# Performance work log

Hardware: AMD Instinct MI355X
Metric: run time of the kernel (lower is better)

The kernel has to match this reference:

```python
import jax, jax.numpy as jnp
import numpy as np

DIM = 1024
H = 16
HD = DIM // H
SCALE = HD ** -0.5
LAMBDA_INIT = 0.1
EPS = 1e-6


def setup_inputs() -> dict:
    key0 = jax.random.key(0)
    ks = jax.random.split(key0, 12)
    B, Nq, Nk = 2, 1024, 2048
    w = 0.02
    inp = {
        "query": jax.random.normal(ks[0], (B, Nq, DIM), jnp.float32),
        "key": jax.random.normal(ks[1], (B, Nk, DIM), jnp.float32),
        "value": jax.random.normal(ks[2], (B, Nk, DIM), jnp.float32),
        "qpos": jax.random.randint(ks[3], (B, Nq), 0, Nq, jnp.int32),
        "kpos": jax.random.randint(ks[4], (B, Nk), 0, Nk, jnp.int32),
        "q1_w": jax.random.normal(ks[5], (DIM, DIM), jnp.float32) * w,
        "q2_w": jax.random.normal(ks[6], (DIM, DIM), jnp.float32) * w,
        "kv1_w": jax.random.normal(ks[7], (2 * DIM, DIM), jnp.float32) * w,
        "kv2_w": jax.random.normal(ks[8], (2 * DIM, DIM), jnp.float32) * w,
        "proj_w": jax.random.normal(ks[9], (DIM, DIM), jnp.float32) * w,
        "proj_b": jnp.zeros((DIM,), jnp.float32),
        "norm_w": jnp.ones((DIM,), jnp.float32),
        "lambda_1": jnp.ones((1, H, 1, 1), jnp.float32),
        # layer_idx=0, max_layer=12 -> scale = 1/12
        "lambda_2": jnp.full((1, H, 1, 1), 1.0 - LAMBDA_INIT * (1.0 / 12.0), jnp.float32),
    }
    return inp


def _split_heads(x, B, N):
    # [B, N, DIM] -> [B, H, N, HD]
    return x.reshape(B, N, H, HD).transpose(0, 2, 1, 3)


def reference(query, key, value, qpos, kpos, q1_w, q2_w, kv1_w, kv2_w,
              proj_w, proj_b, norm_w, lambda_1, lambda_2):
    B, Nq, C = query.shape
    Nk = key.shape[1]

    q1 = _split_heads(query @ q1_w.T, B, Nq)
    q2 = _split_heads(query @ q2_w.T, B, Nq)

    kv1 = (key @ kv1_w.T).reshape(B, Nk, 2, H, HD).transpose(2, 0, 3, 1, 4)
    k1, v1 = kv1[0], kv1[1]  # [B, H, Nk, HD]
    kv2 = (key @ kv2_w.T).reshape(B, Nk, 2, H, HD).transpose(2, 0, 3, 1, 4)
    k2 = kv2[0]

    attn1 = jax.nn.softmax(jnp.einsum('bhqd,bhkd->bhqk', q1, k1) * SCALE, axis=-1)
    attn2 = jax.nn.softmax(jnp.einsum('bhqd,bhkd->bhqk', q2, k2) * SCALE, axis=-1)

    lambda_full = lambda_1 - lambda_2 + LAMBDA_INIT  # [1, H, 1, 1]
    diff_attn = attn1 - lambda_full * attn2

    x = jnp.einsum('bhqk,bhkd->bhqd', diff_attn, v1)
    x = x.transpose(0, 2, 1, 3).reshape(B, Nq, C)

    # RMSNorm (computed in float32 like the original)
    xf = x.astype(jnp.float32)
    xf = xf * jax.lax.rsqrt(jnp.mean(xf * xf, axis=-1, keepdims=True) + EPS) * norm_w
    x = xf.astype(x.dtype)

    return x @ proj_w.T + proj_b
```

## Files before the change

kernel.cpp:

```cpp
#include <hip/hip_runtime.h>
#include <cstdint>

typedef unsigned short u16;
typedef __bf16 bf16x8 __attribute__((ext_vector_type(8)));
typedef float f32x4 __attribute__((ext_vector_type(4)));
typedef float f32x16 __attribute__((ext_vector_type(16)));
typedef uint32_t u32x4 __attribute__((ext_vector_type(4)));

#define SCALE_LOG2E (0.125f * 1.44269504088896340736f)

__device__ __forceinline__ u16 f2bf(float f) {
    uint32_t u = __builtin_bit_cast(uint32_t, f);
    u += 0x7fff + ((u >> 16) & 1);
    return (u16)(u >> 16);
}
__device__ __forceinline__ float bf2f(u16 u) {
    return __builtin_bit_cast(float, (uint32_t)u << 16);
}

__device__ __forceinline__ void gload_lds16(const void* g, void* l) {
    __builtin_amdgcn_global_load_lds(
        (__attribute__((address_space(1))) void*)g,
        (__attribute__((address_space(3))) void*)l, 16, 0, 0);
}

__global__ __launch_bounds__(256) void cvt_all(const float* __restrict__ s0,
                                               const float* __restrict__ s1,
                                               const float* __restrict__ s2,
                                               const float* __restrict__ s3,
                                               const float* __restrict__ s4,
                                               const float* __restrict__ s5,
                                               const float* __restrict__ s6,
                                               u16* __restrict__ d0, u16* __restrict__ d1,
                                               u16* __restrict__ d2, u16* __restrict__ d3,
                                               u16* __restrict__ d4) {
    int i = blockIdx.x * 256 + threadIdx.x;
    const float* src;
    u16* dst;
    int off;
    if (i < 524288)       { src = s0; dst = d0; off = i; }
    else if (i < 1572864) { src = s1; dst = d1; off = i - 524288; }
    else if (i < 1835008) { src = s2; dst = d2; off = i - 1572864; }
    else if (i < 2097152) { src = s3; dst = d2 + (size_t)1024 * 1024; off = i - 1835008; }
    else if (i < 2621440) { src = s4; dst = d3; off = i - 2097152; }
    else if (i < 2883584) { src = s5; dst = d3 + (size_t)2048 * 1024; off = i - 2621440; }
    else                  { src = s6; dst = d4; off = i - 2883584; }
    float4 v = ((const float4*)src)[off];
    ushort4 o;
    o.x = f2bf(v.x); o.y = f2bf(v.y); o.z = f2bf(v.z); o.w = f2bf(v.w);
    ((ushort4*)dst)[off] = o;
}

__global__ __launch_bounds__(256) void gemm_qkv(const u16* __restrict__ Xq,
                                                const u16* __restrict__ Wq,
                                                const u16* __restrict__ Xk,
                                                const u16* __restrict__ Wkv,
                                                u16* __restrict__ q1s, u16* __restrict__ q2s,
                                                u16* __restrict__ k1s, u16* __restrict__ v1t,
                                                u16* __restrict__ k2s) {
    __shared__ u16 As[128 * 32];
    __shared__ u16 Bs[128 * 32];
    const int K = 1024;
    const int bid = blockIdx.x;
    int mode, bm, bn;
    const u16 *A, *B;
    if (bid < 256) {
        mode = 0; bm = bid >> 4; bn = bid & 15; A = Xq; B = Wq;
    } else {
        int t = bid - 256;
        mode = 1; bm = t / 24; bn = t % 24; A = Xk; B = Wkv;
    }
    const int tid = threadIdx.x;
    const int l = tid & 63, w = tid >> 6;
    const int c = l & 15, g = l >> 4;
    const int wr = w >> 1, wc = w & 1;

    f32x4 acc[4][4];
#pragma unroll
    for (int i = 0; i < 4; i++)
#pragma unroll
        for (int j = 0; j < 4; j++) acc[i][j] = f32x4{0.f, 0.f, 0.f, 0.f};

    const u16* Abase = A + (size_t)(bm * 128) * K;
    const u16* Bbase = B + (size_t)(bn * 128) * K;
    const int r0 = 32 * w + (l >> 2);
    const int ch = (l & 3) * 8;

    for (int kb = 0; kb < K; kb += 32) {
        gload_lds16(Abase + (size_t)r0 * K + kb + ch,        As + 32 * w * 32);
        gload_lds16(Abase + (size_t)(r0 + 16) * K + kb + ch, As + (32 * w + 16) * 32);
        gload_lds16(Bbase + (size_t)r0 * K + kb + ch,        Bs + 32 * w * 32);
        gload_lds16(Bbase + (size_t)(r0 + 16) * K + kb + ch, Bs + (32 * w + 16) * 32);
        __syncthreads();
        bf16x8 af[4], bfr[4];
#pragma unroll
        for (int mi = 0; mi < 4; mi++)
            af[mi] = *(const bf16x8*)&As[(64 * wr + 16 * mi + c) * 32 + 8 * g];
#pragma unroll
        for (int ni = 0; ni < 4; ni++)
            bfr[ni] = *(const bf16x8*)&Bs[(64 * wc + 16 * ni + c) * 32 + 8 * g];
#pragma unroll
        for (int mi = 0; mi < 4; mi++)
#pragma unroll
            for (int ni = 0; ni < 4; ni++)
                acc[mi][ni] = __builtin_amdgcn_mfma_f32_16x16x32_bf16(
                    af[mi], bfr[ni], acc[mi][ni], 0, 0, 0);
        __syncthreads();
    }

#pragma unroll
    for (int mi = 0; mi < 4; mi++)
#pragma unroll
        for (int ni = 0; ni < 4; ni++)
#pragma unroll
            for (int j = 0; j < 4; j++) {
                int m = bm * 128 + 64 * wr + 16 * mi + 4 * g + j;
                int n = bn * 128 + 64 * wc + 16 * ni + c;
                float v = acc[mi][ni][j];
                if (mode == 0) {
                    int b = m >> 10, nq = m & 1023;
                    int half = n >> 10, nn = n & 1023;
                    int h = nn >> 6, hd = nn & 63;
                    u16* dst = half ? q2s : q1s;
                    dst[(size_t)((b * 16 + h) * 1024 + nq) * 64 + hd] = f2bf(v * SCALE_LOG2E);
                } else {
                    int b = m >> 11, nk = m & 2047;
                    if (n < 1024) {
                        int h = n >> 6, hd = n & 63;
                        k1s[(size_t)((b * 16 + h) * 2048 + nk) * 64 + hd] = f2bf(v);
                    } else if (n < 2048) {
                        int nn = n - 1024, h = nn >> 6, hd = nn & 63;
                        v1t[(size_t)((b * 16 + h) * 64 + hd) * 2048 + nk] = f2bf(v);
                    } else {
                        int nn = n - 2048, h = nn >> 6, hd = nn & 63;
                        k2s[(size_t)((b * 16 + h) * 2048 + nk) * 64 + hd] = f2bf(v);
                    }
                }
            }
}

__global__ __launch_bounds__(256) void gemm_proj(const u16* __restrict__ A,
                                                 const u16* __restrict__ B,
                                                 float* __restrict__ fo,
                                                 const float* __restrict__ bias) {
    __shared__ u16 As[128 * 32];
    __shared__ u16 Bs[64 * 32];
    const int K = 1024;
    const int bm = blockIdx.x >> 4, bn = blockIdx.x & 15;
    const int tid = threadIdx.x;
    const int l = tid & 63, w = tid >> 6;
    const int c = l & 15, g = l >> 4;
    const int wr = w >> 1, wc = w & 1;

    f32x4 acc[4][2];
#pragma unroll
    for (int i = 0; i < 4; i++)
#pragma unroll
        for (int j = 0; j < 2; j++) acc[i][j] = f32x4{0.f, 0.f, 0.f, 0.f};

    const u16* Abase = A + (size_t)(bm * 128) * K;
    const u16* Bbase = B + (size_t)(bn * 64) * K;
    const int rA = 32 * w + (l >> 2);
    const int rB = 16 * w + (l >> 2);
    const int ch = (l & 3) * 8;

    for (int kb = 0; kb < K; kb += 32) {
        gload_lds16(Abase + (size_t)rA * K + kb + ch,        As + 32 * w * 32);
        gload_lds16(Abase + (size_t)(rA + 16) * K + kb + ch, As + (32 * w + 16) * 32);
        gload_lds16(Bbase + (size_t)rB * K + kb + ch,        Bs + 16 * w * 32);
        __syncthreads();
        bf16x8 af[4], bfr[2];
#pragma unroll
        for (int mi = 0; mi < 4; mi++)
            af[mi] = *(const bf16x8*)&As[(64 * wr + 16 * mi + c) * 32 + 8 * g];
#pragma unroll
        for (int ni = 0; ni < 2; ni++)
            bfr[ni] = *(const bf16x8*)&Bs[(32 * wc + 16 * ni + c) * 32 + 8 * g];
#pragma unroll
        for (int mi = 0; mi < 4; mi++)
#pragma unroll
            for (int ni = 0; ni < 2; ni++)
                acc[mi][ni] = __builtin_amdgcn_mfma_f32_16x16x32_bf16(
                    af[mi], bfr[ni], acc[mi][ni], 0, 0, 0);
        __syncthreads();
    }

#pragma unroll
    for (int mi = 0; mi < 4; mi++)
#pragma unroll
        for (int ni = 0; ni < 2; ni++)
#pragma unroll
            for (int j = 0; j < 4; j++) {
                int m = bm * 128 + 64 * wr + 16 * mi + 4 * g + j;
                int n = bn * 64 + 32 * wc + 16 * ni + c;
                fo[(size_t)m * 1024 + n] = acc[mi][ni][j] + bias[n];
            }
}

__global__ __launch_bounds__(256) void attn_kernel(const u16* __restrict__ q1s,
                                                   const u16* __restrict__ q2s,
                                                   const u16* __restrict__ k1s,
                                                   const u16* __restrict__ k2s,
                                                   const u16* __restrict__ v1t,
                                                   u16* __restrict__ Opart,
                                                   float* __restrict__ Lpart) {
    const int tid = threadIdx.x;
    const int l = tid & 63, w = tid >> 6;
    const int c5 = l & 31, hf = l >> 5;
    const int bid = blockIdx.x;
    const int xcd = bid & 7, slot = bid >> 3;
    const int bh = xcd * 4 + (slot >> 5);
    const int r = slot & 31;
    const int qt = r >> 2, s = r & 3;
    const int b = bh >> 4, head = bh & 15;
    const int q0 = qt * 128 + w * 32;

    bf16x8 qB1[4], qB2[4];
    {
        const u16* p1 = q1s + (size_t)(bh * 1024 + q0 + c5) * 64 + 8 * hf;
        const u16* p2 = q2s + (size_t)(bh * 1024 + q0 + c5) * 64 + 8 * hf;
#pragma unroll
        for (int d = 0; d < 4; d++) {
            qB1[d] = *(const bf16x8*)(p1 + 16 * d);
            qB2[d] = *(const bf16x8*)(p2 + 16 * d);
        }
    }

    f32x16 O1[2], O2[2];
#pragma unroll
    for (int dh = 0; dh < 2; dh++)
#pragma unroll
        for (int i = 0; i < 16; i++) { O1[dh][i] = 0.f; O2[dh][i] = 0.f; }
    float la1 = 0.f, la2 = 0.f;

    const u16* k1b = k1s + (size_t)bh * 2048 * 64 + 8 * hf;
    const u16* k2b = k2s + (size_t)bh * 2048 * 64 + 8 * hf;
    const u16* vb  = v1t + (size_t)bh * 64 * 2048 + 8 * hf;

    const int kb0 = s * 512;
    for (int it = 0; it < 16; it++) {
        const int kb = kb0 + it * 32;
        bf16x8 kA1[4], kA2[4];
        {
            const u16* p1 = k1b + (size_t)(kb + c5) * 64;
            const u16* p2 = k2b + (size_t)(kb + c5) * 64;
#pragma unroll
            for (int d = 0; d < 4; d++) {
                kA1[d] = *(const bf16x8*)(p1 + 16 * d);
                kA2[d] = *(const bf16x8*)(p2 + 16 * d);
            }
        }
        bf16x8 vB[2][2];
#pragma unroll
        for (int dh = 0; dh < 2; dh++)
#pragma unroll
            for (int kk = 0; kk < 2; kk++)
                vB[dh][kk] = *(const bf16x8*)(vb + (size_t)(dh * 32 + c5) * 2048 + kb + kk * 16);

        {
            f32x16 S;
#pragma unroll
            for (int i = 0; i < 16; i++) S[i] = 0.f;
#pragma unroll
            for (int d = 0; d < 4; d++)
                S = __builtin_amdgcn_mfma_f32_32x32x16_bf16(kA1[d], qB1[d], S, 0, 0, 0);
            uint32_t dpk[8];
#pragma unroll
            for (int i = 0; i < 8; i++) {
                float pa = __builtin_exp2f(S[2 * i]);
                float pb = __builtin_exp2f(S[2 * i + 1]);
                la1 += pa + pb;
                asm("v_cvt_pk_bf16_f32 %0, %1, %2" : "=v"(dpk[i]) : "v"(pa), "v"(pb));
            }
            uint32_t a0 = dpk[0], b0 = dpk[2], a1 = dpk[1], b1 = dpk[3];
            asm("v_permlane32_swap_b32 %0, %1" : "+v"(a0), "+v"(b0));
            asm("v_permlane32_swap_b32 %0, %1" : "+v"(a1), "+v"(b1));
            u32x4 t0 = {a0, a1, b0, b1};
            bf16x8 pf0 = __builtin_bit_cast(bf16x8, t0);
            uint32_t a2 = dpk[4], b2 = dpk[6], a3 = dpk[5], b3 = dpk[7];
            asm("v_permlane32_swap_b32 %0, %1" : "+v"(a2), "+v"(b2));
            asm("v_permlane32_swap_b32 %0, %1" : "+v"(a3), "+v"(b3));
            u32x4 t1 = {a2, a3, b2, b3};
            bf16x8 pf1 = __builtin_bit_cast(bf16x8, t1);
#pragma unroll
            for (int dh = 0; dh < 2; dh++) {
                O1[dh] = __builtin_amdgcn_mfma_f32_32x32x16_bf16(pf0, vB[dh][0], O1[dh], 0, 0, 0);
                O1[dh] = __builtin_amdgcn_mfma_f32_32x32x16_bf16(pf1, vB[dh][1], O1[dh], 0, 0, 0);
            }
        }
        {
            f32x16 S;
#pragma unroll
            for (int i = 0; i < 16; i++) S[i] = 0.f;
#pragma unroll
            for (int d = 0; d < 4; d++)
                S = __builtin_amdgcn_mfma_f32_32x32x16_bf16(kA2[d], qB2[d], S, 0, 0, 0);
            uint32_t dpk[8];
#pragma unroll
            for (int i = 0; i < 8; i++) {
                float pa = __builtin_exp2f(S[2 * i]);
                float pb = __builtin_exp2f(S[2 * i + 1]);
                la2 += pa + pb;
                asm("v_cvt_pk_bf16_f32 %0, %1, %2" : "=v"(dpk[i]) : "v"(pa), "v"(pb));
            }
            uint32_t a0 = dpk[0], b0 = dpk[2], a1 = dpk[1], b1 = dpk[3];
            asm("v_permlane32_swap_b32 %0, %1" : "+v"(a0), "+v"(b0));
            asm("v_permlane32_swap_b32 %0, %1" : "+v"(a1), "+v"(b1));
            u32x4 t0 = {a0, a1, b0, b1};
            bf16x8 pf0 = __builtin_bit_cast(bf16x8, t0);
            uint32_t a2 = dpk[4], b2 = dpk[6], a3 = dpk[5], b3 = dpk[7];
            asm("v_permlane32_swap_b32 %0, %1" : "+v"(a2), "+v"(b2));
            asm("v_permlane32_swap_b32 %0, %1" : "+v"(a3), "+v"(b3));
            u32x4 t1 = {a2, a3, b2, b3};
            bf16x8 pf1 = __builtin_bit_cast(bf16x8, t1);
#pragma unroll
            for (int dh = 0; dh < 2; dh++) {
                O2[dh] = __builtin_amdgcn_mfma_f32_32x32x16_bf16(pf0, vB[dh][0], O2[dh], 0, 0, 0);
                O2[dh] = __builtin_amdgcn_mfma_f32_32x32x16_bf16(pf1, vB[dh][1], O2[dh], 0, 0, 0);
            }
        }
    }

    la1 += __shfl_xor(la1, 32, 64);
    la2 += __shfl_xor(la2, 32, 64);

#pragma unroll
    for (int dh = 0; dh < 2; dh++)
#pragma unroll
        for (int rr = 0; rr < 16; rr++) {
            int qrow = (rr & 3) + 8 * (rr >> 2) + 4 * hf;
            size_t rowg = (size_t)b * 1024 + q0 + qrow;
            size_t col = head * 64 + dh * 32 + c5;
            Opart[((size_t)(s * 2 + 0) * 2048 + rowg) * 1024 + col] = f2bf(O1[dh][rr]);
            Opart[((size_t)(s * 2 + 1) * 2048 + rowg) * 1024 + col] = f2bf(O2[dh][rr]);
        }
    if (hf == 0) {
        size_t rowg = (size_t)b * 1024 + q0 + c5;
        Lpart[((size_t)(s * 2 + 0) * 2048 + rowg) * 16 + head] = la1;
        Lpart[((size_t)(s * 2 + 1) * 2048 + rowg) * 16 + head] = la2;
    }
}

__global__ __launch_bounds__(256) void combine_rms(const u16* __restrict__ Opart,
                                                   const float* __restrict__ Lpart,
                                                   const float* __restrict__ lam1,
                                                   const float* __restrict__ lam2,
                                                   const float* __restrict__ nw,
                                                   u16* __restrict__ xn) {
    const int row = blockIdx.x, t = threadIdx.x;
    const int h = t >> 4;
    float a1[4] = {0.f, 0.f, 0.f, 0.f}, a2[4] = {0.f, 0.f, 0.f, 0.f};
    float li1 = 0.f, li2 = 0.f;
#pragma unroll
    for (int s = 0; s < 4; s++) {
        ushort4 u1 = ((const ushort4*)(Opart + ((size_t)(s * 2 + 0) * 2048 + row) * 1024))[t];
        ushort4 u2 = ((const ushort4*)(Opart + ((size_t)(s * 2 + 1) * 2048 + row) * 1024))[t];
        a1[0] += bf2f(u1.x); a1[1] += bf2f(u1.y); a1[2] += bf2f(u1.z); a1[3] += bf2f(u1.w);
        a2[0] += bf2f(u2.x); a2[1] += bf2f(u2.y); a2[2] += bf2f(u2.z); a2[3] += bf2f(u2.w);
        li1 += Lpart[((size_t)(s * 2 + 0) * 2048 + row) * 16 + h];
        li2 += Lpart[((size_t)(s * 2 + 1) * 2048 + row) * 16 + h];
    }
    float lam = lam1[h] - lam2[h] + 0.1f;
    float i1 = 1.0f / li1, i2 = lam / li2;
    float x0 = a1[0] * i1 - a2[0] * i2;
    float x1 = a1[1] * i1 - a2[1] * i2;
    float x2 = a1[2] * i1 - a2[2] * i2;
    float x3 = a1[3] * i1 - a2[3] * i2;
    float ss = x0 * x0 + x1 * x1 + x2 * x2 + x3 * x3;
#pragma unroll
    for (int off = 1; off < 64; off <<= 1) ss += __shfl_xor(ss, off, 64);
    __shared__ float ws4[4];
    if ((t & 63) == 0) ws4[t >> 6] = ss;
    __syncthreads();
    float tot = ws4[0] + ws4[1] + ws4[2] + ws4[3];
    float rs = rsqrtf(tot * (1.0f / 1024.0f) + 1e-6f);
    float4 wv = ((const float4*)nw)[t];
    ushort4 o;
    o.x = f2bf(x0 * rs * wv.x);
    o.y = f2bf(x1 * rs * wv.y);
    o.z = f2bf(x2 * rs * wv.z);
    o.w = f2bf(x3 * rs * wv.w);
    ((ushort4*)(xn + (size_t)row * 1024))[t] = o;
}

extern "C" void kernel_launch(void* const* d_in, const int* in_sizes, int n_in,
                              void* d_out, int out_size, void* d_ws, size_t ws_size,
                              hipStream_t stream) {
    const float* query  = (const float*)d_in[0];
    const float* key    = (const float*)d_in[1];
    const float* q1_w   = (const float*)d_in[5];
    const float* q2_w   = (const float*)d_in[6];
    const float* kv1_w  = (const float*)d_in[7];
    const float* kv2_w  = (const float*)d_in[8];
    const float* proj_w = (const float*)d_in[9];
    const float* proj_b = (const float*)d_in[10];
    const float* norm_w = (const float*)d_in[11];
    const float* lam1   = (const float*)d_in[12];
    const float* lam2   = (const float*)d_in[13];
    float* out = (float*)d_out;

    char* ws = (char*)d_ws;
    size_t off = 0;
    auto alloc = [&](size_t bytes) {
        void* p = ws + off;
        off += (bytes + 255) & ~(size_t)255;
        return p;
    };
    u16* Xq   = (u16*)alloc((size_t)2048 * 1024 * 2);
    u16* Xk   = (u16*)alloc((size_t)4096 * 1024 * 2);
    u16* Wq   = (u16*)alloc((size_t)2048 * 1024 * 2);
    u16* Wkv  = (u16*)alloc((size_t)3072 * 1024 * 2);
    u16* Wp   = (u16*)alloc((size_t)1024 * 1024 * 2);
    u16* q1sb = (u16*)alloc((size_t)32 * 1024 * 64 * 2);
    u16* q2sb = (u16*)alloc((size_t)32 * 1024 * 64 * 2);
    u16* k1sb = (u16*)alloc((size_t)32 * 2048 * 64 * 2);
    u16* k2sb = (u16*)alloc((size_t)32 * 2048 * 64 * 2);
    u16* v1tb = (u16*)alloc((size_t)32 * 64 * 2048 * 2);
    u16* Opart = (u16*)alloc((size_t)8 * 2048 * 1024 * 2);
    float* Lpart = (float*)alloc((size_t)8 * 2048 * 16 * 4);
    u16* xn   = (u16*)alloc((size_t)2048 * 1024 * 2);

    cvt_all<<<12288, 256, 0, stream>>>(query, key, q1_w, q2_w, kv1_w, kv2_w, proj_w,
                                       Xq, Xk, Wq, Wkv, Wp);

    gemm_qkv<<<1024, 256, 0, stream>>>(Xq, Wq, Xk, Wkv, q1sb, q2sb, k1sb, v1tb, k2sb);

    attn_kernel<<<1024, 256, 0, stream>>>(q1sb, q2sb, k1sb, k2sb, v1tb, Opart, Lpart);

    combine_rms<<<2048, 256, 0, stream>>>(Opart, Lpart, lam1, lam2, norm_w, xn);

    gemm_proj<<<256, 256, 0, stream>>>(xn, Wp, out, proj_b);
}
```

Before: 303.6 us.

## Store K1/K2/V1 in MFMA-fragment-major layout for contiguous attention loads

The QKV GEMM epilogue now writes K1, K2 and V1 in a layout where each MFMA operand fragment for a 32-key tile is a contiguous 512-element block indexed by lane. The attention kernel then issues fully coalesced 16-byte-per-lane loads instead of row-strided gathers, especially for the transposed V loads with a 2048-element stride. The cost is more scattered stores in the GEMM epilogue, which were already scattered to some degree.

```diff
diff --git a/kernel.cpp b/kernel.cpp
--- a/kernel.cpp
+++ b/kernel.cpp
@@ -56,8 +56,8 @@
                                                 const u16* __restrict__ Xk,
                                                 const u16* __restrict__ Wkv,
                                                 u16* __restrict__ q1s, u16* __restrict__ q2s,
-                                                u16* __restrict__ k1s, u16* __restrict__ v1t,
-                                                u16* __restrict__ k2s) {
+                                                u16* __restrict__ k1f, u16* __restrict__ v1f,
+                                                u16* __restrict__ k2f) {
     __shared__ u16 As[128 * 32];
     __shared__ u16 Bs[128 * 32];
     const int K = 1024;
@@ -127,13 +127,22 @@
                     int b = m >> 11, nk = m & 2047;
                     if (n < 1024) {
                         int h = n >> 6, hd = n & 63;
-                        k1s[(size_t)((b * 16 + h) * 2048 + nk) * 64 + hd] = f2bf(v);
+                        int bh = b * 16 + h;
+                        size_t idx = ((size_t)(bh * 64 + (nk >> 5)) * 4 + (hd >> 4)) * 512
+                                   + (((hd >> 3) & 1) * 32 + (nk & 31)) * 8 + (hd & 7);
+                        k1f[idx] = f2bf(v);
                     } else if (n < 2048) {
                         int nn = n - 1024, h = nn >> 6, hd = nn & 63;
-                        v1t[(size_t)((b * 16 + h) * 64 + hd) * 2048 + nk] = f2bf(v);
+                        int bh = b * 16 + h;
+                        size_t idx = ((size_t)(bh * 128 + (nk >> 4)) * 2 + (hd >> 5)) * 512
+                                   + (((nk >> 3) & 1) * 32 + (hd & 31)) * 8 + (nk & 7);
+                        v1f[idx] = f2bf(v);
                     } else {
                         int nn = n - 2048, h = nn >> 6, hd = nn & 63;
-                        k2s[(size_t)((b * 16 + h) * 2048 + nk) * 64 + hd] = f2bf(v);
+                        int bh = b * 16 + h;
+                        size_t idx = ((size_t)(bh * 64 + (nk >> 5)) * 4 + (hd >> 4)) * 512
+                                   + (((hd >> 3) & 1) * 32 + (nk & 31)) * 8 + (hd & 7);
+                        k2f[idx] = f2bf(v);
                     }
                 }
             }
@@ -199,9 +208,9 @@
 
 __global__ __launch_bounds__(256) void attn_kernel(const u16* __restrict__ q1s,
                                                    const u16* __restrict__ q2s,
-                                                   const u16* __restrict__ k1s,
-                                                   const u16* __restrict__ k2s,
-                                                   const u16* __restrict__ v1t,
+                                                   const u16* __restrict__ k1fm,
+                                                   const u16* __restrict__ k2fm,
+                                                   const u16* __restrict__ v1fm,
                                                    u16* __restrict__ Opart,
                                                    float* __restrict__ Lpart) {
     const int tid = threadIdx.x;
@@ -233,29 +242,28 @@
         for (int i = 0; i < 16; i++) { O1[dh][i] = 0.f; O2[dh][i] = 0.f; }
     float la1 = 0.f, la2 = 0.f;
 
-    const u16* k1b = k1s + (size_t)bh * 2048 * 64 + 8 * hf;
-    const u16* k2b = k2s + (size_t)bh * 2048 * 64 + 8 * hf;
-    const u16* vb  = v1t + (size_t)bh * 64 * 2048 + 8 * hf;
-
-    const int kb0 = s * 512;
+    const u16* k1t = k1fm + (size_t)bh * 64 * 2048;
+    const u16* k2t = k2fm + (size_t)bh * 64 * 2048;
+    const u16* vt  = v1fm + (size_t)bh * 128 * 1024;
+
     for (int it = 0; it < 16; it++) {
-        const int kb = kb0 + it * 32;
+        const int t32 = s * 16 + it;
+        const u16* p1 = k1t + (size_t)t32 * 2048 + l * 8;
+        const u16* p2 = k2t + (size_t)t32 * 2048 + l * 8;
+        const u16* pv = vt + (size_t)t32 * 2048 + l * 8;
+
         bf16x8 kA1[4], kA2[4];
-        {
-            const u16* p1 = k1b + (size_t)(kb + c5) * 64;
-            const u16* p2 = k2b + (size_t)(kb + c5) * 64;
-#pragma unroll
-            for (int d = 0; d < 4; d++) {
-                kA1[d] = *(const bf16x8*)(p1 + 16 * d);
-                kA2[d] = *(const bf16x8*)(p2 + 16 * d);
-            }
+#pragma unroll
+        for (int d = 0; d < 4; d++) {
+            kA1[d] = *(const bf16x8*)(p1 + d * 512);
+            kA2[d] = *(const bf16x8*)(p2 + d * 512);
         }
         bf16x8 vB[2][2];
 #pragma unroll
-        for (int dh = 0; dh < 2; dh++)
-#pragma unroll
-            for (int kk = 0; kk < 2; kk++)
-                vB[dh][kk] = *(const bf16x8*)(vb + (size_t)(dh * 32 + c5) * 2048 + kb + kk * 16);
+        for (int kk = 0; kk < 2; kk++)
+#pragma unroll
+            for (int dh = 0; dh < 2; dh++)
+                vB[dh][kk] = *(const bf16x8*)(pv + (2 * kk + dh) * 512);
 
         {
             f32x16 S;
@@ -413,9 +421,9 @@
     u16* Wp   = (u16*)alloc((size_t)1024 * 1024 * 2);
     u16* q1sb = (u16*)alloc((size_t)32 * 1024 * 64 * 2);
     u16* q2sb = (u16*)alloc((size_t)32 * 1024 * 64 * 2);
-    u16* k1sb = (u16*)alloc((size_t)32 * 2048 * 64 * 2);
-    u16* k2sb = (u16*)alloc((size_t)32 * 2048 * 64 * 2);
-    u16* v1tb = (u16*)alloc((size_t)32 * 64 * 2048 * 2);
+    u16* k1fb = (u16*)alloc((size_t)32 * 2048 * 64 * 2);
+    u16* k2fb = (u16*)alloc((size_t)32 * 2048 * 64 * 2);
+    u16* v1fb = (u16*)alloc((size_t)32 * 64 * 2048 * 2);
     u16* Opart = (u16*)alloc((size_t)8 * 2048 * 1024 * 2);
     float* Lpart = (float*)alloc((size_t)8 * 2048 * 16 * 4);
     u16* xn   = (u16*)alloc((size_t)2048 * 1024 * 2);
@@ -423,9 +431,9 @@
     cvt_all<<<12288, 256, 0, stream>>>(query, key, q1_w, q2_w, kv1_w, kv2_w, proj_w,
                                        Xq, Xk, Wq, Wkv, Wp);
 
-    gemm_qkv<<<1024, 256, 0, stream>>>(Xq, Wq, Xk, Wkv, q1sb, q2sb, k1sb, v1tb, k2sb);
-
-    attn_kernel<<<1024, 256, 0, stream>>>(q1sb, q2sb, k1sb, k2sb, v1tb, Opart, Lpart);
+    gemm_qkv<<<1024, 256, 0, stream>>>(Xq, Wq, Xk, Wkv, q1sb, q2sb, k1fb, v1fb, k2fb);
+
+    attn_kernel<<<1024, 256, 0, stream>>>(q1sb, q2sb, k1fb, k2fb, v1fb, Opart, Lpart);
 
     combine_rms<<<2048, 256, 0, stream>>>(Opart, Lpart, lam1, lam2, norm_w, xn);
 
```

Result: faster. 266.7 us (-12.2%).
